# Optimization experiments

Measured on AMD Instinct MI355X. Metric: run time of the kernel, lower is better.

The kernel has to match this reference:

```python
import jax, jax.numpy as jnp
import numpy as np

N_NODES = 100000   # nodes per node type
N_EDGES = 800000   # edges per edge type
F_IN = 128         # lazy (-1,-1) input feature dim, chosen == hidden
HID = 128          # hidden_channels
OUT = 1            # out_channels
N_LAYERS = 2
B = 256            # batch_size (num graphs)
NEG_SLOPE = 0.2    # GATConv default leaky_relu slope


def setup_inputs() -> dict:
    key = jax.random.key(0)
    ks = jax.random.split(key, 16)
    x_i = jax.random.normal(ks[0], (N_NODES, F_IN), jnp.float32)
    x_j = jax.random.normal(ks[1], (N_NODES, F_IN), jnp.float32)
    ei_ii = jax.random.randint(ks[2], (2, N_EDGES), 0, N_NODES, jnp.int32)
    ei_jj = jax.random.randint(ks[3], (2, N_EDGES), 0, N_NODES, jnp.int32)
    ei_ij = jax.random.randint(ks[4], (2, N_EDGES), 0, N_NODES, jnp.int32)
    ei_ji = jax.random.randint(ks[5], (2, N_EDGES), 0, N_NODES, jnp.int32)
    batch_i = jnp.sort(jax.random.randint(ks[6], (N_NODES,), 0, B, jnp.int32))
    batch_j = jnp.sort(jax.random.randint(ks[7], (N_NODES,), 0, B, jnp.int32))
    s = 1.0 / np.sqrt(HID)
    Ws = jax.random.normal(ks[8], (N_LAYERS, 4, F_IN, HID), jnp.float32) * s
    Wd = jax.random.normal(ks[9], (N_LAYERS, 4, F_IN, HID), jnp.float32) * s
    att_s = jax.random.normal(ks[10], (N_LAYERS, 4, HID), jnp.float32) * s
    att_d = jax.random.normal(ks[11], (N_LAYERS, 4, HID), jnp.float32) * s
    bias = jnp.zeros((N_LAYERS, 4, HID), jnp.float32)
    lin_w = jax.random.normal(ks[12], (HID, OUT), jnp.float32) * s
    lin_b = jnp.zeros((OUT,), jnp.float32)
    return dict(x_i=x_i, x_j=x_j, ei_ii=ei_ii, ei_jj=ei_jj, ei_ij=ei_ij,
                ei_ji=ei_ji, batch_i=batch_i, batch_j=batch_j, Ws=Ws, Wd=Wd,
                att_s=att_s, att_d=att_d, bias=bias, lin_w=lin_w, lin_b=lin_b)


def gat_conv(x_src, x_dst, edge, W_s, W_d, a_s, a_d, b):
    """Single-head GATConv: gather -> edge attention -> segment softmax -> scatter."""
    src, dst = edge[0], edge[1]
    n_dst = x_dst.shape[0]
    hs = x_src @ W_s                      # [Ns, C]
    hd = x_dst @ W_d                      # [Nd, C]
    e = jax.nn.leaky_relu((hs * a_s).sum(-1)[src] + (hd * a_d).sum(-1)[dst],
                          NEG_SLOPE)      # [E]
    m = jax.ops.segment_max(e, dst, num_segments=n_dst)
    m = jnp.where(jnp.isfinite(m), m, 0.0)  # empty segments -> 0
    p = jnp.exp(e - m[dst])
    denom = jax.ops.segment_sum(p, dst, num_segments=n_dst)
    alpha = p / jnp.maximum(denom[dst], 1e-16)
    out = jax.ops.segment_sum(alpha[:, None] * hs[src], dst, num_segments=n_dst)
    return out + b


def mean_pool(x, batch, size):
    s = jax.ops.segment_sum(x, batch, num_segments=size)
    cnt = jax.ops.segment_sum(jnp.ones((x.shape[0],), x.dtype), batch,
                              num_segments=size)
    return s / jnp.maximum(cnt, 1.0)[:, None]


def reference(x_i, x_j, ei_ii, ei_jj, ei_ij, ei_ji, batch_i, batch_j,
              Ws, Wd, att_s, att_d, bias, lin_w, lin_b):
    xi, xj = x_i, x_j
    for l in range(N_LAYERS):
        # edge-type order: 0=inner_i, 1=inner_j, 2=outer_ij, 3=outer_ji
        out_i = (gat_conv(xi, xi, ei_ii, Ws[l, 0], Wd[l, 0], att_s[l, 0], att_d[l, 0], bias[l, 0])
                 + gat_conv(xj, xi, ei_ji, Ws[l, 3], Wd[l, 3], att_s[l, 3], att_d[l, 3], bias[l, 3]))
        out_j = (gat_conv(xj, xj, ei_jj, Ws[l, 1], Wd[l, 1], att_s[l, 1], att_d[l, 1], bias[l, 1])
                 + gat_conv(xi, xj, ei_ij, Ws[l, 2], Wd[l, 2], att_s[l, 2], att_d[l, 2], bias[l, 2]))
        xi, xj = jnp.tanh(out_i), jnp.tanh(out_j)
    p_i = mean_pool(xi, batch_i, B)       # [B, HID]
    p_j = mean_pool(xj, batch_j, B)       # [B, HID]
    x = 0.5 * (p_i + p_j)                 # mean over the stacked pair
    return jax.nn.sigmoid(x @ lin_w + lin_b)
```

## Files before the change

### kernel.cpp

```cpp
#include <hip/hip_runtime.h>


#define NEG_SLOPE 0.2f

typedef __attribute__((ext_vector_type(8))) short short8v;
typedef __attribute__((ext_vector_type(4))) float float4v;

__device__ __forceinline__ unsigned short f2bf(float f) {
  unsigned u = __float_as_uint(f);
  unsigned r = (u + 0x7FFFu + ((u >> 16) & 1u)) >> 16;
  return (unsigned short)r;
}
__device__ __forceinline__ unsigned pack2(float a, float b) {
  return (unsigned)f2bf(a) | ((unsigned)f2bf(b) << 16);
}
__device__ __forceinline__ float bflo(unsigned u) {
  return __uint_as_float(u << 16);
}
__device__ __forceinline__ float bfhi(unsigned u) {
  return __uint_as_float(u & 0xFFFF0000u);
}
__device__ __forceinline__ float rl_f(float x, int lane) {
  return __int_as_float(__builtin_amdgcn_readlane(__float_as_int(x), lane));
}
__device__ __forceinline__ int rl_i(int x, int lane) {
  return __builtin_amdgcn_readlane(x, lane);
}

__global__ __launch_bounds__(256) void w_to_bf16t(const float* __restrict__ W,
                                                  unsigned short* __restrict__ Wt) {
  __shared__ float buf[64][129];
  int b = blockIdx.x, t = threadIdx.x;
  const float* w = W + (size_t)b * 16384;
  unsigned short* o = Wt + (size_t)b * 16384;
  for (int h = 0; h < 2; ++h) {
    for (int i = 0; i < 32; ++i) {
      int idx = i * 256 + t;
      buf[idx >> 7][idx & 127] = w[(size_t)(h * 64 + (idx >> 7)) * 128 + (idx & 127)];
    }
    __syncthreads();
    for (int i = 0; i < 32; ++i) {
      int idx = i * 256 + t;
      o[(size_t)(idx >> 6) * 128 + h * 64 + (idx & 63)] = f2bf(buf[idx & 63][idx >> 6]);
    }
    __syncthreads();
  }
}

__global__ void precompute_wa(const float* __restrict__ W,
                              const float* __restrict__ att,
                              float* __restrict__ out) {
  int idx = blockIdx.x;
  int f = threadIdx.x;
  const float* w = W + (size_t)idx * 128 * 128 + (size_t)f * 128;
  const float* a = att + idx * 128;
  float s = 0.f;
  #pragma unroll 8
  for (int h = 0; h < 128; ++h) s += w[h] * a[h];
  out[idx * 128 + f] = s;
}

template <int XBF16>
__global__ __launch_bounds__(256) void gemm_dual(
    const void* __restrict__ Xv,
    const unsigned short* __restrict__ Wt1, const float* __restrict__ att1,
    unsigned short* __restrict__ Hb1, float* __restrict__ as1,
    const unsigned short* __restrict__ Wt2, const float* __restrict__ att2,
    unsigned short* __restrict__ Hb2, float* __restrict__ as2,
    const float* __restrict__ vdA, const float* __restrict__ vdB,
    float* __restrict__ adA, float* __restrict__ adB, int M) {
  __shared__ unsigned short Xt[64][136];
  __shared__ unsigned short Wt[128][136];
  const int t = threadIdx.x;
  const int row0 = blockIdx.x * 64;

  {
    int r = t >> 2;
    int cq = (t & 3) * 32;
    int gr = row0 + r;
    if (gr >= M) gr = M - 1;
    if (XBF16) {
      const unsigned short* Xb = (const unsigned short*)Xv;
      const uint4* src = (const uint4*)(Xb + (size_t)gr * 128 + cq);
      #pragma unroll
      for (int i = 0; i < 4; ++i) *(uint4*)&Xt[r][cq + i * 8] = src[i];
    } else {
      const float* Xf = (const float*)Xv;
      const float4* src = (const float4*)(Xf + (size_t)gr * 128 + cq);
      #pragma unroll
      for (int i = 0; i < 8; ++i) {
        float4 v = src[i];
        uint2 u;
        u.x = pack2(v.x, v.y);
        u.y = pack2(v.z, v.w);
        *(uint2*)&Xt[r][cq + i * 4] = u;
      }
    }
  }
  {
    int n = t >> 1;
    int kh = (t & 1) * 64;
    const uint4* src = (const uint4*)(Wt1 + (size_t)n * 128 + kh);
    #pragma unroll
    for (int i = 0; i < 8; ++i) *(uint4*)&Wt[n][kh + i * 8] = src[i];
  }
  __syncthreads();

  if (t < 128) {
    int r = t & 63;
    const float* vd = (t < 64) ? vdA : vdB;
    float* adout = (t < 64) ? adA : adB;
    float sum = 0.f;
    #pragma unroll 4
    for (int k8 = 0; k8 < 16; ++k8) {
      uint4 u = *(const uint4*)&Xt[r][k8 * 8];
      const float* v = vd + k8 * 8;
      sum = fmaf(bflo(u.x), v[0], sum);
      sum = fmaf(bfhi(u.x), v[1], sum);
      sum = fmaf(bflo(u.y), v[2], sum);
      sum = fmaf(bfhi(u.y), v[3], sum);
      sum = fmaf(bflo(u.z), v[4], sum);
      sum = fmaf(bfhi(u.z), v[5], sum);
      sum = fmaf(bflo(u.w), v[6], sum);
      sum = fmaf(bfhi(u.w), v[7], sum);
    }
    int gr = row0 + r;
    if (gr < M) adout[gr] = sum;
  }

  const int lane = t & 63;
  const int wv = t >> 6;
  const int m = lane & 15;
  const int g = lane >> 4;
  const int ws = wv * 16;

  for (int ww = 0; ww < 2; ++ww) {
    if (ww == 1) {
      __syncthreads();
      int n = t >> 1;
      int kh = (t & 1) * 64;
      const uint4* src = (const uint4*)(Wt2 + (size_t)n * 128 + kh);
      #pragma unroll
      for (int i = 0; i < 8; ++i) *(uint4*)&Wt[n][kh + i * 8] = src[i];
      __syncthreads();
    }
    const float* att = ww ? att2 : att1;
    unsigned short* Hb = ww ? Hb2 : Hb1;
    float* as_ = ww ? as2 : as1;

    float4v acc[8];
    float4v z = {0.f, 0.f, 0.f, 0.f};
    #pragma unroll
    for (int nt = 0; nt < 8; ++nt) acc[nt] = z;

    #pragma unroll
    for (int ks = 0; ks < 4; ++ks) {
      short8v a = *(const short8v*)&Xt[ws + m][ks * 32 + g * 8];
      #pragma unroll
      for (int nt = 0; nt < 8; ++nt) {
        short8v b = *(const short8v*)&Wt[nt * 16 + m][ks * 32 + g * 8];
        acc[nt] = __builtin_amdgcn_mfma_f32_16x16x32_bf16(a, b, acc[nt], 0, 0, 0);
      }
    }

    {
      float attv[8];
      #pragma unroll
      for (int nt = 0; nt < 8; ++nt) attv[nt] = att[nt * 16 + m];
      #pragma unroll
      for (int r = 0; r < 4; ++r) {
        float s = 0.f;
        #pragma unroll
        for (int nt = 0; nt < 8; ++nt) s = fmaf(acc[nt][r], attv[nt], s);
        #pragma unroll
        for (int off = 1; off < 16; off <<= 1) s += __shfl_xor(s, off);
        if (m == 0) {
          int grow = row0 + ws + g * 4 + r;
          if (grow < M) as_[grow] = s;
        }
      }
    }

    #pragma unroll
    for (int nt = 0; nt < 8; ++nt) {
      #pragma unroll
      for (int r = 0; r < 4; ++r) {
        float v = acc[nt][r];
        float vn = __shfl_xor(v, 1);
        if ((m & 1) == 0) {
          int grow = row0 + ws + g * 4 + r;
          if (grow < M) {
            *(unsigned*)(Hb + (size_t)grow * 128 + nt * 16 + m) = pack2(v, vn);
          }
        }
      }
    }
  }
}

__global__ void hist4(const int* __restrict__ e0, const int* __restrict__ e1,
                      const int* __restrict__ e2, const int* __restrict__ e3,
                      int E, int* __restrict__ deg, int N) {
  int i = blockIdx.x * 256 + threadIdx.x;
  if (i >= E) return;
  int t = blockIdx.y;
  const int* ei = (t == 0) ? e0 : (t == 1) ? e1 : (t == 2) ? e2 : e3;
  atomicAdd(&deg[t * N + ei[E + i]], 1);
}

__global__ __launch_bounds__(1024) void scan4(const int* __restrict__ deg,
                                              int* __restrict__ rowptr, int N) {
  __shared__ int sums[1024];
  int t = threadIdx.x;
  int ty = blockIdx.x;
  const int* d = deg + (size_t)ty * N;
  int* rp = rowptr + (size_t)ty * (N + 1);
  int chunk = (N + 1023) / 1024;
  int lo = t * chunk;
  int hi = lo + chunk; if (hi > N) hi = N; if (lo > N) lo = N;
  int s = 0;
  for (int i = lo; i < hi; ++i) s += d[i];
  sums[t] = s;
  __syncthreads();
  for (int off = 1; off < 1024; off <<= 1) {
    int add = (t >= off) ? sums[t - off] : 0;
    __syncthreads();
    sums[t] += add;
    __syncthreads();
  }
  int run = (t == 0) ? 0 : sums[t - 1];
  for (int i = lo; i < hi; ++i) {
    rp[i] = run;
    run += d[i];
  }
  if (t == 1023) rp[N] = sums[1023];
}

__global__ void fill4(const int* __restrict__ e0, const int* __restrict__ e1,
                      const int* __restrict__ e2, const int* __restrict__ e3,
                      int E, const int* __restrict__ rowptr,
                      int* __restrict__ fill, int* __restrict__ csrc, int N) {
  int i = blockIdx.x * 256 + threadIdx.x;
  if (i >= E) return;
  int t = blockIdx.y;
  const int* ei = (t == 0) ? e0 : (t == 1) ? e1 : (t == 2) ? e2 : e3;
  int d = ei[E + i];
  int s = ei[i];
  int pos = rowptr[(size_t)t * (N + 1) + d] + atomicAdd(&fill[t * N + d], 1);
  csrc[(size_t)t * E + pos] = s;
}

struct PairArgs {
  const int* rA; const int* sA; const unsigned short* hA;
  const float* asA; const float* adA;
  const int* rB; const int* sB; const unsigned short* hB;
  const float* asB; const float* adB;
  const float* biasA; const float* biasB;
};

__device__ __forceinline__ void agg_pair(const PairArgs& P, int n, int lane,
                                         float2& outA, float2& outB) {
  int begA = P.rA[n], endA = P.rA[n + 1];
  int begB = P.rB[n], endB = P.rB[n + 1];
  float adA = P.adA[n], adB = P.adB[n];
  float lsA = 0.f, lsB = 0.f;
  float2 aA = make_float2(0.f, 0.f), aB = make_float2(0.f, 0.f);
  int cA = begA, cB = begB;
  while (cA < endA || cB < endB) {
    int kA = cA + lane, kB = cB + lane;
    bool vA = kA < endA;
    bool vB = kB < endB;
    int sA = vA ? P.sA[kA] : 0;
    int sB = vB ? P.sB[kB] : 0;
    float eA = vA ? (P.asA[sA] + adA) : 0.f;
    float eB = vB ? (P.asB[sB] + adB) : 0.f;
    eA = eA > 0.f ? eA : NEG_SLOPE * eA;
    eB = eB > 0.f ? eB : NEG_SLOPE * eB;
    float pA = vA ? __expf(eA) : 0.f;
    float pB = vB ? __expf(eB) : 0.f;
    int cntA = endA - cA; cntA = cntA < 0 ? 0 : (cntA > 64 ? 64 : cntA);
    int cntB = endB - cB; cntB = cntB < 0 ? 0 : (cntB > 64 ? 64 : cntB);
    int cnt = cntA > cntB ? cntA : cntB;
    for (int base = 0; base < cnt; base += 8) {
      float qa0 = rl_f(pA, base + 0), qa1 = rl_f(pA, base + 1);
      float qa2 = rl_f(pA, base + 2), qa3 = rl_f(pA, base + 3);
      float qa4 = rl_f(pA, base + 4), qa5 = rl_f(pA, base + 5);
      float qa6 = rl_f(pA, base + 6), qa7 = rl_f(pA, base + 7);
      float qb0 = rl_f(pB, base + 0), qb1 = rl_f(pB, base + 1);
      float qb2 = rl_f(pB, base + 2), qb3 = rl_f(pB, base + 3);
      float qb4 = rl_f(pB, base + 4), qb5 = rl_f(pB, base + 5);
      float qb6 = rl_f(pB, base + 6), qb7 = rl_f(pB, base + 7);
      int ta0 = rl_i(sA, base + 0), ta1 = rl_i(sA, base + 1);
      int ta2 = rl_i(sA, base + 2), ta3 = rl_i(sA, base + 3);
      int ta4 = rl_i(sA, base + 4), ta5 = rl_i(sA, base + 5);
      int ta6 = rl_i(sA, base + 6), ta7 = rl_i(sA, base + 7);
      int tb0 = rl_i(sB, base + 0), tb1 = rl_i(sB, base + 1);
      int tb2 = rl_i(sB, base + 2), tb3 = rl_i(sB, base + 3);
      int tb4 = rl_i(sB, base + 4), tb5 = rl_i(sB, base + 5);
      int tb6 = rl_i(sB, base + 6), tb7 = rl_i(sB, base + 7);
      unsigned ua0 = *(const unsigned*)(P.hA + (size_t)ta0 * 128 + lane * 2);
      unsigned ua1 = *(const unsigned*)(P.hA + (size_t)ta1 * 128 + lane * 2);
      unsigned ua2 = *(const unsigned*)(P.hA + (size_t)ta2 * 128 + lane * 2);
      unsigned ua3 = *(const unsigned*)(P.hA + (size_t)ta3 * 128 + lane * 2);
      unsigned ua4 = *(const unsigned*)(P.hA + (size_t)ta4 * 128 + lane * 2);
      unsigned ua5 = *(const unsigned*)(P.hA + (size_t)ta5 * 128 + lane * 2);
      unsigned ua6 = *(const unsigned*)(P.hA + (size_t)ta6 * 128 + lane * 2);
      unsigned ua7 = *(const unsigned*)(P.hA + (size_t)ta7 * 128 + lane * 2);
      unsigned ub0 = *(const unsigned*)(P.hB + (size_t)tb0 * 128 + lane * 2);
      unsigned ub1 = *(const unsigned*)(P.hB + (size_t)tb1 * 128 + lane * 2);
      unsigned ub2 = *(const unsigned*)(P.hB + (size_t)tb2 * 128 + lane * 2);
      unsigned ub3 = *(const unsigned*)(P.hB + (size_t)tb3 * 128 + lane * 2);
      unsigned ub4 = *(const unsigned*)(P.hB + (size_t)tb4 * 128 + lane * 2);
      unsigned ub5 = *(const unsigned*)(P.hB + (size_t)tb5 * 128 + lane * 2);
      unsigned ub6 = *(const unsigned*)(P.hB + (size_t)tb6 * 128 + lane * 2);
      unsigned ub7 = *(const unsigned*)(P.hB + (size_t)tb7 * 128 + lane * 2);
      lsA += ((qa0 + qa1) + (qa2 + qa3)) + ((qa4 + qa5) + (qa6 + qa7));
      lsB += ((qb0 + qb1) + (qb2 + qb3)) + ((qb4 + qb5) + (qb6 + qb7));
      aA.x = fmaf(qa0, bflo(ua0), aA.x); aA.y = fmaf(qa0, bfhi(ua0), aA.y);
      aA.x = fmaf(qa1, bflo(ua1), aA.x); aA.y = fmaf(qa1, bfhi(ua1), aA.y);
      aA.x = fmaf(qa2, bflo(ua2), aA.x); aA.y = fmaf(qa2, bfhi(ua2), aA.y);
      aA.x = fmaf(qa3, bflo(ua3), aA.x); aA.y = fmaf(qa3, bfhi(ua3), aA.y);
      aA.x = fmaf(qa4, bflo(ua4), aA.x); aA.y = fmaf(qa4, bfhi(ua4), aA.y);
      aA.x = fmaf(qa5, bflo(ua5), aA.x); aA.y = fmaf(qa5, bfhi(ua5), aA.y);
      aA.x = fmaf(qa6, bflo(ua6), aA.x); aA.y = fmaf(qa6, bfhi(ua6), aA.y);
      aA.x = fmaf(qa7, bflo(ua7), aA.x); aA.y = fmaf(qa7, bfhi(ua7), aA.y);
      aB.x = fmaf(qb0, bflo(ub0), aB.x); aB.y = fmaf(qb0, bfhi(ub0), aB.y);
      aB.x = fmaf(qb1, bflo(ub1), aB.x); aB.y = fmaf(qb1, bfhi(ub1), aB.y);
      aB.x = fmaf(qb2, bflo(ub2), aB.x); aB.y = fmaf(qb2, bfhi(ub2), aB.y);
      aB.x = fmaf(qb3, bflo(ub3), aB.x); aB.y = fmaf(qb3, bfhi(ub3), aB.y);
      aB.x = fmaf(qb4, bflo(ub4), aB.x); aB.y = fmaf(qb4, bfhi(ub4), aB.y);
      aB.x = fmaf(qb5, bflo(ub5), aB.x); aB.y = fmaf(qb5, bfhi(ub5), aB.y);
      aB.x = fmaf(qb6, bflo(ub6), aB.x); aB.y = fmaf(qb6, bfhi(ub6), aB.y);
      aB.x = fmaf(qb7, bflo(ub7), aB.x); aB.y = fmaf(qb7, bfhi(ub7), aB.y);
    }
    cA += 64;
    cB += 64;
  }
  float invA = 1.f / fmaxf(lsA, 1e-16f);
  float invB = 1.f / fmaxf(lsB, 1e-16f);
  outA = make_float2(aA.x * invA, aA.y * invA);
  outB = make_float2(aB.x * invB, aB.y * invB);
}

__global__ __launch_bounds__(256) void agg_store2(
    PairArgs P0, unsigned short* __restrict__ out0,
    PairArgs P1, unsigned short* __restrict__ out1, int N) {
  int wave = (blockIdx.x * 256 + threadIdx.x) >> 6;
  int lane = threadIdx.x & 63;
  if (wave >= N) return;
  const PairArgs& P = blockIdx.y ? P1 : P0;
  unsigned short* out = blockIdx.y ? out1 : out0;
  float2 a, b;
  agg_pair(P, wave, lane, a, b);
  float2 b1 = *(const float2*)(P.biasA + lane * 2);
  float2 b2 = *(const float2*)(P.biasB + lane * 2);
  float vx = tanhf(a.x + b.x + b1.x + b2.x);
  float vy = tanhf(a.y + b.y + b1.y + b2.y);
  *(unsigned*)(out + (size_t)wave * 128 + lane * 2) = pack2(vx, vy);
}

__global__ __launch_bounds__(256) void agg_pool2(
    PairArgs P0, const int* __restrict__ batch0, float* __restrict__ pool0,
    PairArgs P1, const int* __restrict__ batch1, float* __restrict__ pool1,
    int N) {
  int wave = (blockIdx.x * 256 + threadIdx.x) >> 6;
  int lane = threadIdx.x & 63;
  if (wave >= N) return;
  const PairArgs& P = blockIdx.y ? P1 : P0;
  const int* batch = blockIdx.y ? batch1 : batch0;
  float* pool = blockIdx.y ? pool1 : pool0;
  float2 a, b;
  agg_pair(P, wave, lane, a, b);
  float2 b1 = *(const float2*)(P.biasA + lane * 2);
  float2 b2 = *(const float2*)(P.biasB + lane * 2);
  float vx = tanhf(a.x + b.x + b1.x + b2.x);
  float vy = tanhf(a.y + b.y + b1.y + b2.y);
  int bb = batch[wave];
  float* p = pool + (size_t)bb * 128 + lane * 2;
  unsafeAtomicAdd(p, vx);
  unsafeAtomicAdd(p + 1, vy);
}

__device__ __forceinline__ int lower_bound_i(const int* __restrict__ a, int n,
                                             int v) {
  int lo = 0, hi = n;
  while (lo < hi) {
    int mid = (lo + hi) >> 1;
    if (a[mid] < v) lo = mid + 1; else hi = mid;
  }
  return lo;
}

__global__ void final_k(const float* __restrict__ pool_i,
                        const int* __restrict__ batch_i,
                        const float* __restrict__ pool_j,
                        const int* __restrict__ batch_j, int N,
                        const float* __restrict__ lin_w,
                        const float* __restrict__ lin_b,
                        float* __restrict__ out) {
  int b = threadIdx.x;
  float ci = (float)(lower_bound_i(batch_i, N, b + 1) -
                     lower_bound_i(batch_i, N, b));
  float cj = (float)(lower_bound_i(batch_j, N, b + 1) -
                     lower_bound_i(batch_j, N, b));
  ci = fmaxf(ci, 1.f);
  cj = fmaxf(cj, 1.f);
  float acc = 0.f;
  #pragma unroll 4
  for (int f = 0; f < 128; ++f) {
    float x = 0.5f * (pool_i[(size_t)b * 128 + f] / ci +
                      pool_j[(size_t)b * 128 + f] / cj);
    acc += x * lin_w[f];
  }
  acc += lin_b[0];
  out[b] = 1.f / (1.f + __expf(-acc));
}

extern "C" void kernel_launch(void* const* d_in, const int* in_sizes, int n_in,
                              void* d_out, int out_size, void* d_ws,
                              size_t ws_size, hipStream_t stream) {
  const float* x_i = (const float*)d_in[0];
  const float* x_j = (const float*)d_in[1];
  const int* ei_arr[4] = {(const int*)d_in[2], (const int*)d_in[3],
                          (const int*)d_in[4], (const int*)d_in[5]};
  const int* batch_i = (const int*)d_in[6];
  const int* batch_j = (const int*)d_in[7];
  const float* Ws = (const float*)d_in[8];
  const float* Wd = (const float*)d_in[9];
  const float* att_s = (const float*)d_in[10];
  const float* att_d = (const float*)d_in[11];
  const float* bias = (const float*)d_in[12];
  const float* lin_w = (const float*)d_in[13];
  const float* lin_b = (const float*)d_in[14];
  float* out = (float*)d_out;

  const int N = in_sizes[0] / 128;
  const int E = in_sizes[2] / 2;
  const size_t NF = (size_t)N * 128;

  char* w = (char*)d_ws;
  auto alloc = [&](size_t bytes) {
    char* p = w;
    w += (bytes + 255) & ~(size_t)255;
    return p;
  };
  unsigned short* bufA_i = (unsigned short*)alloc(NF * 2);
  unsigned short* bufA_j = (unsigned short*)alloc(NF * 2);
  unsigned short* hsb[4];
  for (int c = 0; c < 4; ++c) hsb[c] = (unsigned short*)alloc(NF * 2);
  int* csrc = (int*)alloc((size_t)4 * E * 4);
  int* rowptr = (int*)alloc((size_t)4 * (N + 1) * 4);
  int* deg = (int*)alloc((size_t)4 * N * 4);
  int* fillc = (int*)alloc((size_t)4 * N * 4);
  float* asb[4];
  for (int c = 0; c < 4; ++c) asb[c] = (float*)alloc((size_t)N * 4);
  float* adb[4];
  for (int c = 0; c < 4; ++c) adb[c] = (float*)alloc((size_t)N * 4);
  float* wdad = (float*)alloc(8 * 128 * 4);
  unsigned short* Wst = (unsigned short*)alloc(8 * 16384 * 2);
  float* pool = (float*)alloc(2 * 256 * 128 * 4);
  float* pool_i = pool;
  float* pool_j = pool + 256 * 128;

  w_to_bf16t<<<8, 256, 0, stream>>>(Ws, Wst);
  precompute_wa<<<8, 128, 0, stream>>>(Wd, att_d, wdad);

  hipMemsetAsync(deg, 0, (size_t)4 * N * 4, stream);
  hipMemsetAsync(fillc, 0, (size_t)4 * N * 4, stream);
  dim3 egrid((E + 255) / 256, 4);
  hist4<<<egrid, 256, 0, stream>>>(ei_arr[0], ei_arr[1], ei_arr[2], ei_arr[3],
                                   E, deg, N);
  scan4<<<4, 1024, 0, stream>>>(deg, rowptr, N);
  fill4<<<egrid, 256, 0, stream>>>(ei_arr[0], ei_arr[1], ei_arr[2], ei_arr[3],
                                   E, rowptr, fillc, csrc, N);

  hipMemsetAsync(pool, 0, 2 * 256 * 128 * 4, stream);

  const int gemm_blocks = (N + 63) / 64;
  const int nodew_blocks = (N + 3) / 4;

  for (int l = 0; l < 2; ++l) {
    const void* cur_i = (l == 0) ? (const void*)x_i : (const void*)bufA_i;
    const void* cur_j = (l == 0) ? (const void*)x_j : (const void*)bufA_j;
    const size_t L = (size_t)l * 4;

    if (l == 0) {
      gemm_dual<0><<<gemm_blocks, 256, 0, stream>>>(
          cur_i, Wst + (L + 0) * 16384, att_s + (L + 0) * 128, hsb[0], asb[0],
          Wst + (L + 2) * 16384, att_s + (L + 2) * 128, hsb[2], asb[2],
          wdad + (L + 0) * 128, wdad + (L + 3) * 128, adb[0], adb[3], N);
      gemm_dual<0><<<gemm_blocks, 256, 0, stream>>>(
          cur_j, Wst + (L + 1) * 16384, att_s + (L + 1) * 128, hsb[1], asb[1],
          Wst + (L + 3) * 16384, att_s + (L + 3) * 128, hsb[3], asb[3],
          wdad + (L + 1) * 128, wdad + (L + 2) * 128, adb[1], adb[2], N);
    } else {
      gemm_dual<1><<<gemm_blocks, 256, 0, stream>>>(
          cur_i, Wst + (L + 0) * 16384, att_s + (L + 0) * 128, hsb[0], asb[0],
          Wst + (L + 2) * 16384, att_s + (L + 2) * 128, hsb[2], asb[2],
          wdad + (L + 0) * 128, wdad + (L + 3) * 128, adb[0], adb[3], N);
      gemm_dual<1><<<gemm_blocks, 256, 0, stream>>>(
          cur_j, Wst + (L + 1) * 16384, att_s + (L + 1) * 128, hsb[1], asb[1],
          Wst + (L + 3) * 16384, att_s + (L + 3) * 128, hsb[3], asb[3],
          wdad + (L + 1) * 128, wdad + (L + 2) * 128, adb[1], adb[2], N);
    }

    PairArgs P0 = {rowptr + (size_t)0 * (N + 1), csrc + (size_t)0 * E, hsb[0],
                   asb[0], adb[0],
                   rowptr + (size_t)3 * (N + 1), csrc + (size_t)3 * E, hsb[3],
                   asb[3], adb[3],
                   bias + (L + 0) * 128, bias + (L + 3) * 128};
    PairArgs P1 = {rowptr + (size_t)1 * (N + 1), csrc + (size_t)1 * E, hsb[1],
                   asb[1], adb[1],
                   rowptr + (size_t)2 * (N + 1), csrc + (size_t)2 * E, hsb[2],
                   asb[2], adb[2],
                   bias + (L + 1) * 128, bias + (L + 2) * 128};

    dim3 agrid(nodew_blocks, 2);
    if (l == 0) {
      agg_store2<<<agrid, 256, 0, stream>>>(P0, bufA_i, P1, bufA_j, N);
    } else {
      agg_pool2<<<agrid, 256, 0, stream>>>(P0, batch_i, pool_i, P1, batch_j,
                                           pool_j, N);
    }
  }

  final_k<<<1, 256, 0, stream>>>(pool_i, batch_i, pool_j, batch_j, N, lin_w,
                                 lin_b, out);
}
```

Measured before the change: 1.109 ms.

## Precompute per-edge attention weights in edge-order pass and merge dual GEMM launches

Adds an edge_p4 kernel that computes the leaky-relu and exp attention weight for each edge in original order and scatters (src, p) pairs into CSR order. The aggregation kernel then reads these packed pairs and no longer does the random as[src] gather or the exp in its inner loop. fill4 now records each edge's CSR position instead of its source index. The two gemm_dual launches per layer are merged into one launch using a 2D grid. In exchange, each layer pays an extra pass over all edges with random scattered writes, and the CSR array doubles in size.

```diff
diff --git a/kernel.cpp b/kernel.cpp
--- a/kernel.cpp
+++ b/kernel.cpp
@@ -60,19 +60,25 @@
   out[idx * 128 + f] = s;
 }
 
+struct GemmArgs {
+  const unsigned short* Wt1; const float* att1;
+  unsigned short* Hb1; float* as1;
+  const unsigned short* Wt2; const float* att2;
+  unsigned short* Hb2; float* as2;
+  const float* vdA; const float* vdB;
+  float* adA; float* adB;
+};
+
 template <int XBF16>
-__global__ __launch_bounds__(256) void gemm_dual(
-    const void* __restrict__ Xv,
-    const unsigned short* __restrict__ Wt1, const float* __restrict__ att1,
-    unsigned short* __restrict__ Hb1, float* __restrict__ as1,
-    const unsigned short* __restrict__ Wt2, const float* __restrict__ att2,
-    unsigned short* __restrict__ Hb2, float* __restrict__ as2,
-    const float* __restrict__ vdA, const float* __restrict__ vdB,
-    float* __restrict__ adA, float* __restrict__ adB, int M) {
+__global__ __launch_bounds__(256) void gemm_dual2(
+    const void* __restrict__ X0, const void* __restrict__ X1,
+    GemmArgs Ga, GemmArgs Gb, int M) {
   __shared__ unsigned short Xt[64][136];
   __shared__ unsigned short Wt[128][136];
   const int t = threadIdx.x;
   const int row0 = blockIdx.x * 64;
+  const void* Xv = blockIdx.y ? X1 : X0;
+  const GemmArgs& G = blockIdx.y ? Gb : Ga;
 
   {
     int r = t >> 2;
@@ -100,7 +106,7 @@
   {
     int n = t >> 1;
     int kh = (t & 1) * 64;
-    const uint4* src = (const uint4*)(Wt1 + (size_t)n * 128 + kh);
+    const uint4* src = (const uint4*)(G.Wt1 + (size_t)n * 128 + kh);
     #pragma unroll
     for (int i = 0; i < 8; ++i) *(uint4*)&Wt[n][kh + i * 8] = src[i];
   }
@@ -108,8 +114,8 @@
 
   if (t < 128) {
     int r = t & 63;
-    const float* vd = (t < 64) ? vdA : vdB;
-    float* adout = (t < 64) ? adA : adB;
+    const float* vd = (t < 64) ? G.vdA : G.vdB;
+    float* adout = (t < 64) ? G.adA : G.adB;
     float sum = 0.f;
     #pragma unroll 4
     for (int k8 = 0; k8 < 16; ++k8) {
@@ -139,14 +145,14 @@
       __syncthreads();
       int n = t >> 1;
       int kh = (t & 1) * 64;
-      const uint4* src = (const uint4*)(Wt2 + (size_t)n * 128 + kh);
+      const uint4* src = (const uint4*)(G.Wt2 + (size_t)n * 128 + kh);
       #pragma unroll
       for (int i = 0; i < 8; ++i) *(uint4*)&Wt[n][kh + i * 8] = src[i];
       __syncthreads();
     }
-    const float* att = ww ? att2 : att1;
-    unsigned short* Hb = ww ? Hb2 : Hb1;
-    float* as_ = ww ? as2 : as1;
+    const float* att = ww ? G.att2 : G.att1;
+    unsigned short* Hb = ww ? G.Hb2 : G.Hb1;
+    float* as_ = ww ? G.as2 : G.as1;
 
     float4v acc[8];
     float4v z = {0.f, 0.f, 0.f, 0.f};
@@ -239,22 +245,42 @@
 __global__ void fill4(const int* __restrict__ e0, const int* __restrict__ e1,
                       const int* __restrict__ e2, const int* __restrict__ e3,
                       int E, const int* __restrict__ rowptr,
-                      int* __restrict__ fill, int* __restrict__ csrc, int N) {
+                      int* __restrict__ fill, int* __restrict__ epos, int N) {
   int i = blockIdx.x * 256 + threadIdx.x;
   if (i >= E) return;
   int t = blockIdx.y;
   const int* ei = (t == 0) ? e0 : (t == 1) ? e1 : (t == 2) ? e2 : e3;
   int d = ei[E + i];
+  int pos = rowptr[(size_t)t * (N + 1) + d] + atomicAdd(&fill[t * N + d], 1);
+  epos[(size_t)t * E + i] = pos;
+}
+
+__global__ void edge_p4(const int* __restrict__ e0, const int* __restrict__ e1,
+                        const int* __restrict__ e2, const int* __restrict__ e3,
+                        int E, const int* __restrict__ epos,
+                        const float* __restrict__ as0, const float* __restrict__ as1,
+                        const float* __restrict__ as2, const float* __restrict__ as3,
+                        const float* __restrict__ ad0, const float* __restrict__ ad1,
+                        const float* __restrict__ ad2, const float* __restrict__ ad3,
+                        uint2* __restrict__ spcsr) {
+  int i = blockIdx.x * 256 + threadIdx.x;
+  if (i >= E) return;
+  int t = blockIdx.y;
+  const int* ei = (t == 0) ? e0 : (t == 1) ? e1 : (t == 2) ? e2 : e3;
+  const float* as_ = (t == 0) ? as0 : (t == 1) ? as1 : (t == 2) ? as2 : as3;
+  const float* ad_ = (t == 0) ? ad0 : (t == 1) ? ad1 : (t == 2) ? ad2 : ad3;
   int s = ei[i];
-  int pos = rowptr[(size_t)t * (N + 1) + d] + atomicAdd(&fill[t * N + d], 1);
-  csrc[(size_t)t * E + pos] = s;
+  int d = ei[E + i];
+  float e = as_[s] + ad_[d];
+  e = e > 0.f ? e : NEG_SLOPE * e;
+  float p = __expf(e);
+  int k = epos[(size_t)t * E + i];
+  spcsr[(size_t)t * E + k] = make_uint2((unsigned)s, __float_as_uint(p));
 }
 
 struct PairArgs {
-  const int* rA; const int* sA; const unsigned short* hA;
-  const float* asA; const float* adA;
-  const int* rB; const int* sB; const unsigned short* hB;
-  const float* asB; const float* adB;
+  const int* rA; const uint2* spA; const unsigned short* hA;
+  const int* rB; const uint2* spB; const unsigned short* hB;
   const float* biasA; const float* biasB;
 };
 
@@ -262,22 +288,17 @@
                                          float2& outA, float2& outB) {
   int begA = P.rA[n], endA = P.rA[n + 1];
   int begB = P.rB[n], endB = P.rB[n + 1];
-  float adA = P.adA[n], adB = P.adB[n];
   float lsA = 0.f, lsB = 0.f;
   float2 aA = make_float2(0.f, 0.f), aB = make_float2(0.f, 0.f);
   int cA = begA, cB = begB;
   while (cA < endA || cB < endB) {
     int kA = cA + lane, kB = cB + lane;
-    bool vA = kA < endA;
-    bool vB = kB < endB;
-    int sA = vA ? P.sA[kA] : 0;
-    int sB = vB ? P.sB[kB] : 0;
-    float eA = vA ? (P.asA[sA] + adA) : 0.f;
-    float eB = vB ? (P.asB[sB] + adB) : 0.f;
-    eA = eA > 0.f ? eA : NEG_SLOPE * eA;
-    eB = eB > 0.f ? eB : NEG_SLOPE * eB;
-    float pA = vA ? __expf(eA) : 0.f;
-    float pB = vB ? __expf(eB) : 0.f;
+    uint2 vAu = (kA < endA) ? P.spA[kA] : make_uint2(0u, 0u);
+    uint2 vBu = (kB < endB) ? P.spB[kB] : make_uint2(0u, 0u);
+    int sA = (int)vAu.x;
+    int sB = (int)vBu.x;
+    float pA = __uint_as_float(vAu.y);
+    float pB = __uint_as_float(vBu.y);
     int cntA = endA - cA; cntA = cntA < 0 ? 0 : (cntA > 64 ? 64 : cntA);
     int cntB = endB - cB; cntB = cntB < 0 ? 0 : (cntB > 64 ? 64 : cntB);
     int cnt = cntA > cntB ? cntA : cntB;
@@ -448,10 +469,11 @@
   unsigned short* bufA_j = (unsigned short*)alloc(NF * 2);
   unsigned short* hsb[4];
   for (int c = 0; c < 4; ++c) hsb[c] = (unsigned short*)alloc(NF * 2);
-  int* csrc = (int*)alloc((size_t)4 * E * 4);
   int* rowptr = (int*)alloc((size_t)4 * (N + 1) * 4);
   int* deg = (int*)alloc((size_t)4 * N * 4);
   int* fillc = (int*)alloc((size_t)4 * N * 4);
+  int* epos = (int*)alloc((size_t)4 * E * 4);
+  uint2* spcsr = (uint2*)alloc((size_t)4 * E * 8);
   float* asb[4];
   for (int c = 0; c < 4; ++c) asb[c] = (float*)alloc((size_t)N * 4);
   float* adb[4];
@@ -472,7 +494,7 @@
                                    E, deg, N);
   scan4<<<4, 1024, 0, stream>>>(deg, rowptr, N);
   fill4<<<egrid, 256, 0, stream>>>(ei_arr[0], ei_arr[1], ei_arr[2], ei_arr[3],
-                                   E, rowptr, fillc, csrc, N);
+                                   E, rowptr, fillc, epos, N);
 
   hipMemsetAsync(pool, 0, 2 * 256 * 128 * 4, stream);
 
@@ -484,35 +506,29 @@
     const void* cur_j = (l == 0) ? (const void*)x_j : (const void*)bufA_j;
     const size_t L = (size_t)l * 4;
 
+    GemmArgs Ga = {Wst + (L + 0) * 16384, att_s + (L + 0) * 128, hsb[0], asb[0],
+                   Wst + (L + 2) * 16384, att_s + (L + 2) * 128, hsb[2], asb[2],
+                   wdad + (L + 0) * 128, wdad + (L + 3) * 128, adb[0], adb[3]};
+    GemmArgs Gb = {Wst + (L + 1) * 16384, att_s + (L + 1) * 128, hsb[1], asb[1],
+                   Wst + (L + 3) * 16384, att_s + (L + 3) * 128, hsb[3], asb[3],
+                   wdad + (L + 1) * 128, wdad + (L + 2) * 128, adb[1], adb[2]};
+    dim3 ggrid(gemm_blocks, 2);
     if (l == 0) {
-      gemm_dual<0><<<gemm_blocks, 256, 0, stream>>>(
-          cur_i, Wst + (L + 0) * 16384, att_s + (L + 0) * 128, hsb[0], asb[0],
-          Wst + (L + 2) * 16384, att_s + (L + 2) * 128, hsb[2], asb[2],
-          wdad + (L + 0) * 128, wdad + (L + 3) * 128, adb[0], adb[3], N);
-      gemm_dual<0><<<gemm_blocks, 256, 0, stream>>>(
-          cur_j, Wst + (L + 1) * 16384, att_s + (L + 1) * 128, hsb[1], asb[1],
-          Wst + (L + 3) * 16384, att_s + (L + 3) * 128, hsb[3], asb[3],
-          wdad + (L + 1) * 128, wdad + (L + 2) * 128, adb[1], adb[2], N);
+      gemm_dual2<0><<<ggrid, 256, 0, stream>>>(cur_i, cur_j, Ga, Gb, N);
     } else {
-      gemm_dual<1><<<gemm_blocks, 256, 0, stream>>>(
-          cur_i, Wst + (L + 0) * 16384, att_s + (L + 0) * 128, hsb[0], asb[0],
-          Wst + (L + 2) * 16384, att_s + (L + 2) * 128, hsb[2], asb[2],
-          wdad + (L + 0) * 128, wdad + (L + 3) * 128, adb[0], adb[3], N);
-      gemm_dual<1><<<gemm_blocks, 256, 0, stream>>>(
-          cur_j, Wst + (L + 1) * 16384, att_s + (L + 1) * 128, hsb[1], asb[1],
-          Wst + (L + 3) * 16384, att_s + (L + 3) * 128, hsb[3], asb[3],
-          wdad + (L + 1) * 128, wdad + (L + 2) * 128, adb[1], adb[2], N);
-    }
-
-    PairArgs P0 = {rowptr + (size_t)0 * (N + 1), csrc + (size_t)0 * E, hsb[0],
-                   asb[0], adb[0],
-                   rowptr + (size_t)3 * (N + 1), csrc + (size_t)3 * E, hsb[3],
-                   asb[3], adb[3],
+      gemm_dual2<1><<<ggrid, 256, 0, stream>>>(cur_i, cur_j, Ga, Gb, N);
+    }
+
+    edge_p4<<<egrid, 256, 0, stream>>>(
+        ei_arr[0], ei_arr[1], ei_arr[2], ei_arr[3], E, epos,
+        asb[0], asb[1], asb[2], asb[3],
+        adb[0], adb[1], adb[2], adb[3], spcsr);
+
+    PairArgs P0 = {rowptr + (size_t)0 * (N + 1), spcsr + (size_t)0 * E, hsb[0],
+                   rowptr + (size_t)3 * (N + 1), spcsr + (size_t)3 * E, hsb[3],
                    bias + (L + 0) * 128, bias + (L + 3) * 128};
-    PairArgs P1 = {rowptr + (size_t)1 * (N + 1), csrc + (size_t)1 * E, hsb[1],
-                   asb[1], adb[1],
-                   rowptr + (size_t)2 * (N + 1), csrc + (size_t)2 * E, hsb[2],
-                   asb[2], adb[2],
+    PairArgs P1 = {rowptr + (size_t)1 * (N + 1), spcsr + (size_t)1 * E, hsb[1],
+                   rowptr + (size_t)2 * (N + 1), spcsr + (size_t)2 * E, hsb[2],
                    bias + (L + 1) * 128, bias + (L + 2) * 128};
 
     dim3 agrid(nodew_blocks, 2);
```

Result: slower. 1.150 ms (+3.7%).
